# Performance work log

Hardware: AMD Instinct MI355X
Metric: run time of the kernel (lower is better)

## Reference

```python
import math
import jax, jax.numpy as jnp
import numpy as np

QDEPTH = 8
WIDTH = 32
HEIGHT = 32
PIXELS = WIDTH * HEIGHT          # 1024
WIRES = int(math.ceil(math.log2(PIXELS)))  # 10, and PIXELS == 2**WIRES exactly
BATCH = 2048


def setup_inputs() -> dict:
    key = jax.random.key(0)
    k1, k2 = jax.random.split(key)
    x = jax.random.normal(k1, (BATCH, 1, WIDTH, HEIGHT), dtype=jnp.float32)
    # torch.randn(weight_shape) * 0.4
    weights = jax.random.normal(k2, (QDEPTH, WIRES, 3), dtype=jnp.float32) * 0.4
    return {"x": x, "weights": weights, "reps": 1}


def _apply_1q(s, U, wire):
    # s: (batch, 2, 2, ..., 2); apply 2x2 unitary U on qubit `wire` (axis wire+1)
    ax = wire + 1
    s = jnp.moveaxis(s, ax, -1)
    s = s @ U.T                      # new[..., i] = sum_j U[i, j] * old[..., j]
    return jnp.moveaxis(s, -1, ax)


def _apply_cnot(s, ctrl, tgt):
    # flip target bit on the control==1 half of the state
    c_ax = ctrl + 1
    t_ax = tgt + 1
    s0 = jnp.take(s, 0, axis=c_ax)
    s1 = jnp.take(s, 1, axis=c_ax)
    t = t_ax - 1 if t_ax > c_ax else t_ax
    s1 = jnp.flip(s1, axis=t)
    return jnp.stack([s0, s1], axis=c_ax)


def _rot_matrix(phi, theta, omega):
    # qml.Rot = RZ(phi) -> RY(theta) -> RZ(omega)
    c = jnp.cos(theta * 0.5)
    sn = jnp.sin(theta * 0.5)
    ep = jnp.exp(-0.5j * (phi + omega))   # e^{-i(phi+omega)/2}
    em = jnp.exp(-0.5j * (phi - omega))   # e^{-i(phi-omega)/2}
    return jnp.stack([
        jnp.stack([ep * c, -jnp.conj(em) * sn]),
        jnp.stack([em * sn, jnp.conj(ep) * c]),
    ]).astype(jnp.complex64)


def _circuit(psi, weights, reps):
    # psi: (batch, 2**WIRES) complex64 normalized state
    b = psi.shape[0]
    s = psi.reshape((b,) + (2,) * WIRES)
    w = jnp.tanh(weights)                 # qw_map.tanh
    # StronglyEntanglingLayers default ranges: r_l = l % (wires-1) + 1
    ranges = [(l % (WIRES - 1)) + 1 for l in range(QDEPTH)]
    for _ in range(reps):
        for l in range(QDEPTH):
            for q in range(WIRES):
                U = _rot_matrix(w[l, q, 0], w[l, q, 1], w[l, q, 2])
                s = _apply_1q(s, U, q)
            r = ranges[l]
            for q in range(WIRES):
                s = _apply_cnot(s, q, (q + r) % WIRES)
    return s.reshape(b, 2 ** WIRES)


def reference(x, weights, reps):
    b = x.shape[0]
    v = x.reshape(b, PIXELS)                       # b 1 w h -> b (w h)
    old_norm = jnp.linalg.norm(v, axis=-1, keepdims=True)
    psi = (v / old_norm).astype(jnp.complex64)     # real amplitudes, zero imag
    out = _circuit(psi, weights, reps)
    out = out * old_norm.astype(jnp.complex64)
    return out.reshape(b, 1, WIDTH, HEIGHT)
```

## Files before the change

kernel.cpp:

```cpp
#include <hip/hip_runtime.h>
#include <math.h>


#define WIRES   10
#define NSTATE  1024
#define QDEPTH  8
#define NBATCH  2048
#define NGATES  (QDEPTH * WIRES)

#define WS_WORDS 1728

__device__ __forceinline__ int perm_g(int j, int r) {
#pragma unroll
    for (int q = WIRES - 1; q >= 0; --q) {
        const int cb = 9 - q;
        const int tb = 9 - ((q + r) % WIRES);
        j ^= ((j >> cb) & 1) << tb;
    }
    return j;
}

__global__ __launch_bounds__(1024) void qprep(
    const float* __restrict__ weights, float* __restrict__ ws)
{
    const int tid = threadIdx.x;
    if (tid < NGATES) {
        const float phi   = tanhf(weights[tid * 3 + 0]);
        const float theta = tanhf(weights[tid * 3 + 1]);
        const float omega = tanhf(weights[tid * 3 + 2]);
        const float c  = cosf(theta * 0.5f);
        const float sn = sinf(theta * 0.5f);
        const float a  = 0.5f * (phi + omega);
        const float bb = 0.5f * (phi - omega);
        const float ca = cosf(a),  sa = sinf(a);
        const float cb = cosf(bb), sb = sinf(bb);
        ws[tid * 8 + 0] =  ca * c;  ws[tid * 8 + 1] = -sa * c;
        ws[tid * 8 + 2] = -cb * sn; ws[tid * 8 + 3] = -sb * sn;
        ws[tid * 8 + 4] =  cb * sn; ws[tid * 8 + 5] = -sb * sn;
        ws[tid * 8 + 6] =  ca * c;  ws[tid * 8 + 7] =  sa * c;
    }
    int* wsI = (int*)ws;
    if (tid < 64) {
        const int l = tid >> 3, t = tid & 7;
        wsI[640 + tid] = perm_g(t, (l % (WIRES - 1)) + 1);
    }
    {
        const int l = tid >> 7, e = tid & 127;
        const int i0 = ((e >> 6) << 9) | ((e & 63) << 3);
        wsI[704 + tid] = perm_g(i0, (l % (WIRES - 1)) + 1);
    }
}

template<int CTRL>
__device__ __forceinline__ float dppmov(float x) {
    return __int_as_float(__builtin_amdgcn_update_dpp(
        0, __float_as_int(x), CTRL, 0xF, 0xF, true));
}
#define FX1(v)  dppmov<0xB1>(v)
#define FX2(v)  dppmov<0x4E>(v)
#define FX4(v)  dppmov<0x1B>(dppmov<0x141>(v))
#define FX8(v)  dppmov<0x128>(v)
#define FX16(v) __shfl_xor((v), 16, 64)
#define FX32(v) __shfl_xor((v), 32, 64)

#define APPLY_LOCAL8(uptr, mask)                                              \
    {                                                                         \
        const float* __restrict__ u = (uptr);                                 \
        const float u00r = u[0], u00i = u[1], u01r = u[2], u01i = u[3];       \
        const float u10r = u[4], u10i = u[5], u11r = u[6], u11i = u[7];       \
        _Pragma("unroll")                                                     \
        for (int t0 = 0; t0 < 8; ++t0) {                                      \
            if (t0 & (mask)) continue;                                        \
            const int t1 = t0 | (mask);                                       \
            const float a0r = re[t0], a0i = im[t0];                           \
            const float a1r = re[t1], a1i = im[t1];                           \
            re[t0] = u00r*a0r - u00i*a0i + u01r*a1r - u01i*a1i;               \
            im[t0] = u00r*a0i + u00i*a0r + u01r*a1i + u01i*a1r;               \
            re[t1] = u10r*a0r - u10i*a0i + u11r*a1r - u11i*a1i;               \
            im[t1] = u10r*a0i + u10i*a0r + u11r*a1i + u11i*a1r;               \
        }                                                                     \
    }

#define LANE_GATE8(W, J, FETCH)                                               \
    {                                                                         \
        const float* __restrict__ u = gw + (W) * 8;                           \
        const bool hi = (lane >> (J)) & 1;                                    \
        const float c0r = hi ? u[6] : u[0], c0i = hi ? u[7] : u[1];           \
        const float c1r = hi ? u[4] : u[2], c1i = hi ? u[5] : u[3];           \
        _Pragma("unroll")                                                     \
        for (int t = 0; t < 8; ++t) {                                         \
            const float pr = FETCH(re[t]);                                    \
            const float pi = FETCH(im[t]);                                    \
            const float sr = re[t], si = im[t];                               \
            re[t] = c0r*sr - c0i*si + c1r*pr - c1i*pi;                        \
            im[t] = c0r*si + c0i*sr + c1r*pi + c1i*pr;                        \
        }                                                                     \
    }

__global__ __launch_bounds__(128) void qsim2(
    const float* __restrict__ x,
    const float* __restrict__ ws,
    float* __restrict__ out,
    const int interleaved)
{
    __shared__ float lre[NSTATE];
    __shared__ float lim[NSTATE];
    const int tid  = threadIdx.x;
    const int lane = tid & 63;
    const int b    = blockIdx.x;
    const int i0   = ((tid >> 6) << 9) | (lane << 3);
    const int* __restrict__ wsI = (const int*)ws;

    float re[8], im[8];

    const float4* __restrict__ x4 =
        (const float4*)(x + ((size_t)b << 10) + i0);
    {
        const float4 v0 = x4[0], v1 = x4[1];
        re[0]=v0.x; re[1]=v0.y; re[2]=v0.z; re[3]=v0.w;
        re[4]=v1.x; re[5]=v1.y; re[6]=v1.z; re[7]=v1.w;
#pragma unroll
        for (int t = 0; t < 8; ++t) im[t] = 0.f;
    }

    for (int l = 0; l < QDEPTH; ++l) {
        const float* __restrict__ gw = ws + l * 80;

        APPLY_LOCAL8(gw + 9*8, 1)
        APPLY_LOCAL8(gw + 8*8, 2)
        APPLY_LOCAL8(gw + 7*8, 4)

        LANE_GATE8(6, 0, FX1)
        LANE_GATE8(5, 1, FX2)
        LANE_GATE8(4, 2, FX4)
        LANE_GATE8(3, 3, FX8)
        LANE_GATE8(2, 4, FX16)
        LANE_GATE8(1, 5, FX32)

        *(float4*)&lre[i0]     = make_float4(re[0], re[1], re[2], re[3]);
        *(float4*)&lre[i0 + 4] = make_float4(re[4], re[5], re[6], re[7]);
        *(float4*)&lim[i0]     = make_float4(im[0], im[1], im[2], im[3]);
        *(float4*)&lim[i0 + 4] = make_float4(im[4], im[5], im[6], im[7]);
        __syncthreads();

        const float* __restrict__ u0 = gw;
        const int gl = wsI[704 + l * 128 + tid];
#pragma unroll
        for (int t = 0; t < 8; ++t) {
            const int j  = gl ^ wsI[640 + l * 8 + t];
            const int jp = j ^ 512;
            const float sr = lre[j],  si = lim[j];
            const float pr = lre[jp], pi = lim[jp];
            const bool hib = (j >> 9) & 1;
            const float c0r = hib ? u0[6] : u0[0], c0i = hib ? u0[7] : u0[1];
            const float c1r = hib ? u0[4] : u0[2], c1i = hib ? u0[5] : u0[3];
            re[t] = c0r*sr - c0i*si + c1r*pr - c1i*pi;
            im[t] = c0r*si + c0i*sr + c1r*pi + c1i*pr;
        }
        __syncthreads();
    }

    if (interleaved) {
        float4* __restrict__ o4 = (float4*)(out + 2 * (((size_t)b << 10) + i0));
        o4[0] = make_float4(re[0], im[0], re[1], im[1]);
        o4[1] = make_float4(re[2], im[2], re[3], im[3]);
        o4[2] = make_float4(re[4], im[4], re[5], im[5]);
        o4[3] = make_float4(re[6], im[6], re[7], im[7]);
    } else {
        float4* __restrict__ o4 = (float4*)(out + ((size_t)b << 10) + i0);
        o4[0] = make_float4(re[0], re[1], re[2], re[3]);
        o4[1] = make_float4(re[4], re[5], re[6], re[7]);
    }
}

__global__ __launch_bounds__(256) void qcircuit_kernel(
    const float* __restrict__ x, const float* __restrict__ weights,
    float* __restrict__ out, const int interleaved)
{
    __shared__ float s_re[NSTATE];
    __shared__ float s_im[NSTATE];
    __shared__ float s_g[NGATES][8];
    const int tid = threadIdx.x;
    const int b   = blockIdx.x;
    if (tid < NGATES) {
        const float phi   = tanhf(weights[tid * 3 + 0]);
        const float theta = tanhf(weights[tid * 3 + 1]);
        const float omega = tanhf(weights[tid * 3 + 2]);
        const float c  = cosf(theta * 0.5f);
        const float sn = sinf(theta * 0.5f);
        const float a  = 0.5f * (phi + omega);
        const float bb = 0.5f * (phi - omega);
        const float ca = cosf(a),  sa = sinf(a);
        const float cb = cosf(bb), sb = sinf(bb);
        s_g[tid][0] =  ca * c;  s_g[tid][1] = -sa * c;
        s_g[tid][2] = -cb * sn; s_g[tid][3] = -sb * sn;
        s_g[tid][4] =  cb * sn; s_g[tid][5] = -sb * sn;
        s_g[tid][6] =  ca * c;  s_g[tid][7] =  sa * c;
    }
#pragma unroll
    for (int k = 0; k < 4; ++k) {
        const int i = tid + 256 * k;
        s_re[i] = x[b * NSTATE + i];
        s_im[i] = 0.0f;
    }
    __syncthreads();
    for (int l = 0; l < QDEPTH; ++l) {
        for (int q = 0; q < WIRES; ++q) {
            const int gi = l * WIRES + q;
            const float u00r = s_g[gi][0], u00i = s_g[gi][1];
            const float u01r = s_g[gi][2], u01i = s_g[gi][3];
            const float u10r = s_g[gi][4], u10i = s_g[gi][5];
            const float u11r = s_g[gi][6], u11i = s_g[gi][7];
            const int sh = 9 - q;
            const int m  = 1 << sh;
#pragma unroll
            for (int k = 0; k < 2; ++k) {
                const int p  = tid + 256 * k;
                const int i0 = ((p >> sh) << (sh + 1)) | (p & (m - 1));
                const int i1 = i0 | m;
                const float a0r = s_re[i0], a0i = s_im[i0];
                const float a1r = s_re[i1], a1i = s_im[i1];
                s_re[i0] = u00r*a0r - u00i*a0i + u01r*a1r - u01i*a1i;
                s_im[i0] = u00r*a0i + u00i*a0r + u01r*a1i + u01i*a1r;
                s_re[i1] = u10r*a0r - u10i*a0i + u11r*a1r - u11i*a1i;
                s_im[i1] = u10r*a0i + u10i*a0r + u11r*a1i + u11i*a1r;
            }
            __syncthreads();
        }
        const int r = (l % (WIRES - 1)) + 1;
        float vr[4], vi[4];
#pragma unroll
        for (int k = 0; k < 4; ++k) {
            const int i = tid + 256 * k;
            const int j = perm_g(i, r);
            vr[k] = s_re[j]; vi[k] = s_im[j];
        }
        __syncthreads();
#pragma unroll
        for (int k = 0; k < 4; ++k) {
            const int i = tid + 256 * k;
            s_re[i] = vr[k]; s_im[i] = vi[k];
        }
        __syncthreads();
    }
    if (interleaved) {
#pragma unroll
        for (int k = 0; k < 4; ++k) {
            const int i  = tid + 256 * k;
            const int fi = 2 * (b * NSTATE + i);
            out[fi + 0] = s_re[i];
            out[fi + 1] = s_im[i];
        }
    } else {
#pragma unroll
        for (int k = 0; k < 4; ++k) {
            const int i = tid + 256 * k;
            out[b * NSTATE + i] = s_re[i];
        }
    }
}

extern "C" void kernel_launch(void* const* d_in, const int* in_sizes, int n_in,
                              void* d_out, int out_size, void* d_ws, size_t ws_size,
                              hipStream_t stream) {
    const float* x       = (const float*)d_in[0];
    const float* weights = (const float*)d_in[1];
    float* out = (float*)d_out;
    const int interleaved = (out_size >= 2 * NBATCH * NSTATE) ? 1 : 0;

    if (ws_size >= WS_WORDS * sizeof(float)) {
        float* ws = (float*)d_ws;
        qprep<<<1, 1024, 0, stream>>>(weights, ws);
        qsim2<<<NBATCH, 128, 0, stream>>>(x, ws, out, interleaved);
    } else {
        qcircuit_kernel<<<NBATCH, 256, 0, stream>>>(x, weights, out, interleaved);
    }
}
```

Before: 108.7 us.

## Transpose shared-memory state layout and double-buffer LDS to drop second barrier

Stores the state in shared memory with a transposed word mapping (index bits rotated so each thread writes stride-128 words), with the precomputed permutation tables converted to the new word index. The shared buffers are double-buffered by layer parity, which removes the trailing __syncthreads per layer. The intent is fewer LDS bank conflicts on the scattered permuted reads and one less barrier per layer, at the cost of scalar instead of float4 LDS stores and twice the shared memory.

```diff
diff --git a/kernel.cpp b/kernel.cpp
--- a/kernel.cpp
+++ b/kernel.cpp
@@ -18,6 +18,9 @@
         j ^= ((j >> cb) & 1) << tb;
     }
     return j;
+}
+__device__ __forceinline__ int wordof(int j) {
+    return ((j & 7) << 7) | (j >> 3);
 }
 
 __global__ __launch_bounds__(1024) void qprep(
@@ -40,14 +43,14 @@
         ws[tid * 8 + 6] =  ca * c;  ws[tid * 8 + 7] =  sa * c;
     }
     int* wsI = (int*)ws;
-    if (tid < 64) {
-        const int l = tid >> 3, t = tid & 7;
-        wsI[640 + tid] = perm_g(t, (l % (WIRES - 1)) + 1);
+    if (tid >= 128 && tid < 192) {
+        const int e = tid - 128, l = e >> 3, t = e & 7;
+        wsI[640 + e] = wordof(perm_g(t, (l % (WIRES - 1)) + 1));
     }
     {
         const int l = tid >> 7, e = tid & 127;
         const int i0 = ((e >> 6) << 9) | ((e & 63) << 3);
-        wsI[704 + tid] = perm_g(i0, (l % (WIRES - 1)) + 1);
+        wsI[704 + tid] = wordof(perm_g(i0, (l % (WIRES - 1)) + 1));
     }
 }
 
@@ -66,8 +69,8 @@
 #define APPLY_LOCAL8(uptr, mask)                                              \
     {                                                                         \
         const float* __restrict__ u = (uptr);                                 \
-        const float u00r = u[0], u00i = u[1], u01r = u[2], u01i = u[3];       \
-        const float u10r = u[4], u10i = u[5], u11r = u[6], u11i = u[7];       \
+        const float u00r=u[0], u00i=u[1], u01r=u[2], u01i=u[3];               \
+        const float u10r=u[4], u10i=u[5], u11r=u[6], u11i=u[7];               \
         _Pragma("unroll")                                                     \
         for (int t0 = 0; t0 < 8; ++t0) {                                      \
             if (t0 & (mask)) continue;                                        \
@@ -103,8 +106,8 @@
     float* __restrict__ out,
     const int interleaved)
 {
-    __shared__ float lre[NSTATE];
-    __shared__ float lim[NSTATE];
+    __shared__ float lre[2][NSTATE];
+    __shared__ float lim[2][NSTATE];
     const int tid  = threadIdx.x;
     const int lane = tid & 63;
     const int b    = blockIdx.x;
@@ -125,6 +128,8 @@
 
     for (int l = 0; l < QDEPTH; ++l) {
         const float* __restrict__ gw = ws + l * 80;
+        float* __restrict__ bre = lre[l & 1];
+        float* __restrict__ bim = lim[l & 1];
 
         APPLY_LOCAL8(gw + 9*8, 1)
         APPLY_LOCAL8(gw + 8*8, 2)
@@ -137,27 +142,27 @@
         LANE_GATE8(2, 4, FX16)
         LANE_GATE8(1, 5, FX32)
 
-        *(float4*)&lre[i0]     = make_float4(re[0], re[1], re[2], re[3]);
-        *(float4*)&lre[i0 + 4] = make_float4(re[4], re[5], re[6], re[7]);
-        *(float4*)&lim[i0]     = make_float4(im[0], im[1], im[2], im[3]);
-        *(float4*)&lim[i0 + 4] = make_float4(im[4], im[5], im[6], im[7]);
+#pragma unroll
+        for (int t = 0; t < 8; ++t) {
+            bre[t * 128 + tid] = re[t];
+            bim[t * 128 + tid] = im[t];
+        }
         __syncthreads();
 
         const float* __restrict__ u0 = gw;
-        const int gl = wsI[704 + l * 128 + tid];
+        const int glw = wsI[704 + l * 128 + tid];
 #pragma unroll
         for (int t = 0; t < 8; ++t) {
-            const int j  = gl ^ wsI[640 + l * 8 + t];
-            const int jp = j ^ 512;
-            const float sr = lre[j],  si = lim[j];
-            const float pr = lre[jp], pi = lim[jp];
-            const bool hib = (j >> 9) & 1;
+            const int jw  = glw ^ wsI[640 + l * 8 + t];
+            const int jpw = jw ^ 64;
+            const float sr = bre[jw],  si = bim[jw];
+            const float pr = bre[jpw], pi = bim[jpw];
+            const bool hib = (jw >> 6) & 1;
             const float c0r = hib ? u0[6] : u0[0], c0i = hib ? u0[7] : u0[1];
             const float c1r = hib ? u0[4] : u0[2], c1i = hib ? u0[5] : u0[3];
             re[t] = c0r*sr - c0i*si + c1r*pr - c1i*pi;
             im[t] = c0r*si + c0i*sr + c1r*pi + c1i*pr;
         }
-        __syncthreads();
     }
 
     if (interleaved) {
```

Result: slower. 115.5 us (+6.3%).
